# Kernel optimization log

Measured on AMD Instinct MI355X. Metric: run time of the kernel, lower is better.

Reference implementation:

```python
import jax, jax.numpy as jnp
import numpy as np

BOS = 1
MAX_LEN = 20


def _lstm_cell(x, h, c, Wih, Whh, bih, bhh):
    # torch.nn.LSTMCell gate order: i, f, g, o
    g = x @ Wih.T + h @ Whh.T + bih + bhh
    i, f, gg, o = jnp.split(g, 4, axis=-1)
    c = jax.nn.sigmoid(f) * c + jax.nn.sigmoid(i) * jnp.tanh(gg)
    h = jax.nn.sigmoid(o) * jnp.tanh(c)
    return h, c


def setup_inputs() -> dict:
    key = jax.random.key(0)
    ks = jax.random.split(key, 12)
    B, K, D = 512, 36, 2048
    A, H, Em, V = 512, 512, 300, 10000
    s = 0.02
    rn = lambda k, shape, sc=s: sc * jax.random.normal(k, shape, dtype=jnp.float32)
    return {
        'feats': jax.random.normal(ks[0], (B, K, D), dtype=jnp.float32),
        'Wp': rn(ks[1], (A, D)), 'bp': jnp.zeros((A,), jnp.float32),
        'E': rn(ks[2], (V, Em), 0.1).at[0].set(0.0),  # padding_idx = 0
        'Wih1': rn(ks[3], (4 * H, Em + A)), 'Whh1': rn(ks[4], (4 * H, H)),
        'bih1': jnp.zeros((4 * H,), jnp.float32), 'bhh1': jnp.zeros((4 * H,), jnp.float32),
        'Wih2': rn(ks[5], (4 * H, H + A)), 'Whh2': rn(ks[6], (4 * H, H)),
        'bih2': jnp.zeros((4 * H,), jnp.float32), 'bhh2': jnp.zeros((4 * H,), jnp.float32),
        'Wa1': rn(ks[7], (A, H + A)), 'ba1': jnp.zeros((A,), jnp.float32),
        'wa2': rn(ks[8], (1, A)), 'ba2': jnp.zeros((1,), jnp.float32),
        'Wo': rn(ks[9], (V, H)), 'bo': jnp.zeros((V,), jnp.float32),
    }


def reference(feats, Wp, bp, E, Wih1, Whh1, bih1, bhh1, Wih2, Whh2, bih2, bhh2,
              Wa1, ba1, wa2, ba2, Wo, bo):
    B, K, D = feats.shape
    H = Whh1.shape[1]
    f_att = feats @ Wp.T + bp                      # [B, K, A]
    f_mean = f_att.mean(axis=1)                    # [B, A]
    # attn Linear over concat([h1, f_att]): split columns, precompute f_att term
    Wa1_h, Wa1_f = Wa1[:, :H], Wa1[:, H:]
    att_f = f_att @ Wa1_f.T + ba1                  # [B, K, A]
    x0 = jnp.broadcast_to(E[BOS], (B, E.shape[1]))
    z = jnp.zeros((B, H), jnp.float32)
    carry0 = (x0, z, z, z, z)

    def step(carry, _):
        x, h1, c1, h2, c2 = carry
        h1, c1 = _lstm_cell(jnp.concatenate([x, f_mean], axis=-1), h1, c1,
                            Wih1, Whh1, bih1, bhh1)
        pre = jnp.tanh(att_f + (h1 @ Wa1_h.T)[:, None, :])   # [B, K, A]
        e = pre @ wa2[0] + ba2[0]                            # [B, K]
        alpha = jax.nn.softmax(e, axis=-1)
        ctx = jnp.einsum('bk,bka->ba', alpha, f_att)         # [B, A]
        h2, c2 = _lstm_cell(jnp.concatenate([h1, ctx], axis=-1), h2, c2,
                            Wih2, Whh2, bih2, bhh2)
        logit = h2 @ Wo.T + bo                               # [B, V]  (dropout is identity in eval)
        nxt = jnp.argmax(logit, axis=-1)
        return (E[nxt], h1, c1, h2, c2), nxt

    _, ids = jax.lax.scan(step, carry0, None, length=MAX_LEN - 1)
    return ids.T  # [B, MAX_LEN-1], matches torch.stack(out_ids, 1)
```

## Files before the change

### kernel.cpp

```cpp
#include <hip/hip_runtime.h>
#include <math.h>
#include <stdint.h>

constexpr int Bsz = 512, Kf = 36, Dd = 2048, Aa = 512, Hh = 512, Em = 300;
constexpr int Vv = 10000, TSTEPS = 19, BOS = 1;
constexpr int K1 = 832;
constexpr int K2 = 1536;
constexpr int VvP = 10112;
constexpr float SPLIT_S  = 2048.0f;
constexpr float SPLIT_IS = 1.0f / 2048.0f;

#define CDIV(a,b) (((a)+(b)-1)/(b))

typedef _Float16 f16x8 __attribute__((ext_vector_type(8)));
typedef float    f32x4 __attribute__((ext_vector_type(4)));

typedef const unsigned int GU __attribute__((address_space(1)));
typedef unsigned int       LU __attribute__((address_space(3)));

__device__ __forceinline__ void gload16(const void* g, void* l) {
    __builtin_amdgcn_global_load_lds((GU*)g, (LU*)l, 16, 0, 0);
}

template<int N> __device__ __forceinline__ void wait_vm() {
    if constexpr (N == 0)       asm volatile("s_waitcnt vmcnt(0)" ::: "memory");
    else if constexpr (N == 4)  asm volatile("s_waitcnt vmcnt(4)" ::: "memory");
    else if constexpr (N == 6)  asm volatile("s_waitcnt vmcnt(6)" ::: "memory");
    else if constexpr (N == 8)  asm volatile("s_waitcnt vmcnt(8)" ::: "memory");
    else if constexpr (N == 12) asm volatile("s_waitcnt vmcnt(12)" ::: "memory");
    else if constexpr (N == 16) asm volatile("s_waitcnt vmcnt(16)" ::: "memory");
    else static_assert(N == 0, "unsupported vmcnt literal");
}
#define WAIT_LGKM asm volatile("s_waitcnt lgkmcnt(0)" ::: "memory")
#define SB0 __builtin_amdgcn_sched_barrier(0)
#define BAR __builtin_amdgcn_s_barrier()

__device__ __forceinline__ float sigm(float v) { return 1.0f / (1.0f + expf(-v)); }

__device__ __forceinline__ void wsplit(_Float16* __restrict__ hi, _Float16* __restrict__ lo,
                                       size_t idx, float v) {
    _Float16 h = (_Float16)v;
    hi[idx] = h;
    lo[idx] = (_Float16)((v - (float)h) * SPLIT_S);
}

template<int BM, int BN, int BK, bool AF32>
__global__ __launch_bounds__(256)
void gemm_sp(const float* __restrict__ Af,
             const _Float16* __restrict__ Ahi, const _Float16* __restrict__ Alo, int lda,
             const _Float16* __restrict__ Bhi, const _Float16* __restrict__ Blo, int ldb,
             float* __restrict__ C, int ldc, int N, int K,
             const float* __restrict__ bias1, const float* __restrict__ bias2,
             const float* __restrict__ addC)
{
    constexpr int WM = BM / 2, WN = BN / 2;
    constexpr int MF = WM / 16, NF = WN / 16;
    constexpr int PA  = BK / 8;
    constexpr int PSA = BM * 8 + 8;
    constexpr int PSB = BN * 8 + 8;
    constexpr int SZA = PA * PSA, SZB = PA * PSB;
    constexpr int OAH = 0, OAL = SZA, OBH = 2 * SZA, OBL = 2 * SZA + SZB;
    constexpr int BUF = 2 * SZA + 2 * SZB;
    constexpr int NCHA = BM * BK / 2048;
    constexpr int NCHB = BN * BK / 2048;
    constexpr int LW = 2 * NCHA + 2 * NCHB;
    __shared__ _Float16 sm[2 * BUF];

    const int t    = threadIdx.x;
    const int lane = t & 63;
    const int w    = t >> 6;
    const int wr   = w >> 1, wc = w & 1;
    const int m0   = blockIdx.y * BM, n0 = blockIdx.x * BN;
    const int l15  = lane & 15, l4 = lane >> 4;

    f32x4 acch[MF][NF];
    f32x4 accm[MF][NF];
    #pragma unroll
    for (int m = 0; m < MF; ++m)
        #pragma unroll
        for (int n = 0; n < NF; ++n) {
            acch[m][n] = (f32x4){0.f, 0.f, 0.f, 0.f};
            accm[m][n] = (f32x4){0.f, 0.f, 0.f, 0.f};
        }

    const int nkt = K / BK;

    auto stageB = [&](int bufo, int kt) {
        #pragma unroll
        for (int i = 0; i < NCHB; ++i) {
            const int q  = i * 256 + t;
            const int p  = q / BN, r = q % BN;
            const int qw = i * 256 + (t & ~63);
            const int pu = qw / BN, ru = qw % BN;
            const size_t goff = (size_t)(n0 + r) * ldb + kt * BK + p * 8;
            gload16(Bhi + goff, &sm[bufo + OBH + pu * PSB + ru * 8]);
            gload16(Blo + goff, &sm[bufo + OBL + pu * PSB + ru * 8]);
        }
    };
    auto stageA16 = [&](int bufo, int kt) {
        #pragma unroll
        for (int i = 0; i < NCHA; ++i) {
            const int q  = i * 256 + t;
            const int p  = q / BM, r = q % BM;
            const int qw = i * 256 + (t & ~63);
            const int pu = qw / BM, ru = qw % BM;
            const size_t goff = (size_t)(m0 + r) * lda + kt * BK + p * 8;
            gload16(Ahi + goff, &sm[bufo + OAH + pu * PSA + ru * 8]);
            gload16(Alo + goff, &sm[bufo + OAL + pu * PSA + ru * 8]);
        }
    };
    auto issueA = [&](float4 (&rd)[NCHA][2], int kt) {
        #pragma unroll
        for (int i = 0; i < NCHA; ++i) {
            const int q = i * 256 + t;
            const int p = q / BM, r = q % BM;
            const float* src = Af + (size_t)(m0 + r) * lda + kt * BK + p * 8;
            rd[i][0] = *(const float4*)src;
            rd[i][1] = *(const float4*)(src + 4);
        }
    };
    auto writeA = [&](int bufo, float4 (&rd)[NCHA][2]) {
        #pragma unroll
        for (int i = 0; i < NCHA; ++i) {
            const int q = i * 256 + t;
            const int p = q / BM, r = q % BM;
            const float f[8] = {rd[i][0].x, rd[i][0].y, rd[i][0].z, rd[i][0].w,
                                rd[i][1].x, rd[i][1].y, rd[i][1].z, rd[i][1].w};
            f16x8 hi, lo;
            #pragma unroll
            for (int j = 0; j < 8; ++j) {
                _Float16 h = (_Float16)f[j];
                hi[j] = h;
                lo[j] = (_Float16)((f[j] - (float)h) * SPLIT_S);
            }
            *(f16x8*)&sm[bufo + OAH + p * PSA + r * 8] = hi;
            *(f16x8*)&sm[bufo + OAL + p * PSA + r * 8] = lo;
        }
    };
    auto compute = [&](int bufo) {
        #pragma unroll
        for (int s = 0; s < BK / 32; ++s) {
            f16x8 ah[MF], al[MF], bh[NF], bl[NF];
            const int pl = s * 4 + l4;
            #pragma unroll
            for (int m = 0; m < MF; ++m) {
                const int row = wr * WM + m * 16 + l15;
                ah[m] = *(const f16x8*)&sm[bufo + OAH + pl * PSA + row * 8];
                al[m] = *(const f16x8*)&sm[bufo + OAL + pl * PSA + row * 8];
            }
            #pragma unroll
            for (int n = 0; n < NF; ++n) {
                const int row = wc * WN + n * 16 + l15;
                bh[n] = *(const f16x8*)&sm[bufo + OBH + pl * PSB + row * 8];
                bl[n] = *(const f16x8*)&sm[bufo + OBL + pl * PSB + row * 8];
            }
            #pragma unroll
            for (int m = 0; m < MF; ++m)
                #pragma unroll
                for (int n = 0; n < NF; ++n) {
                    acch[m][n] = __builtin_amdgcn_mfma_f32_16x16x32_f16(ah[m], bh[n], acch[m][n], 0, 0, 0);
                    accm[m][n] = __builtin_amdgcn_mfma_f32_16x16x32_f16(ah[m], bl[n], accm[m][n], 0, 0, 0);
                    accm[m][n] = __builtin_amdgcn_mfma_f32_16x16x32_f16(al[m], bh[n], accm[m][n], 0, 0, 0);
                }
        }
    };

    if constexpr (AF32) {
        float4 rA[NCHA][2], rB[NCHA][2];
        issueA(rA, 0); stageB(0, 0);
        for (int kt = 0; kt < nkt; kt += 2) {
            issueA(rB, kt + 1); stageB(BUF, kt + 1);
            wait_vm<LW>(); SB0;
            writeA(0, rA);
            WAIT_LGKM; SB0;
            BAR; SB0;
            compute(0);
            SB0; WAIT_LGKM; BAR; SB0;
            if (kt + 2 < nkt) { issueA(rA, kt + 2); stageB(0, kt + 2); wait_vm<LW>(); }
            else              { wait_vm<0>(); }
            SB0;
            writeA(BUF, rB);
            WAIT_LGKM; SB0;
            BAR; SB0;
            compute(BUF);
            SB0; WAIT_LGKM; BAR; SB0;
        }
    } else {
        stageA16(0, 0); stageB(0, 0);
        for (int kt = 0; kt < nkt; ++kt) {
            const int bufc = (kt & 1) ? BUF : 0;
            const int bufn = BUF - bufc;
            if (kt + 1 < nkt) { stageA16(bufn, kt + 1); stageB(bufn, kt + 1); wait_vm<LW>(); }
            else              { wait_vm<0>(); }
            SB0;
            BAR; SB0;
            compute(bufc);
            SB0; WAIT_LGKM; BAR; SB0;
        }
    }

    #pragma unroll
    for (int m = 0; m < MF; ++m) {
        const int rowb = m0 + wr * WM + m * 16 + l4 * 4;
        #pragma unroll
        for (int n = 0; n < NF; ++n) {
            const int col = n0 + wc * WN + n * 16 + l15;
            if (col < N) {
                float bb = 0.f;
                if (bias1) bb += bias1[col];
                if (bias2) bb += bias2[col];
                #pragma unroll
                for (int r = 0; r < 4; ++r) {
                    const size_t idx = (size_t)(rowb + r) * ldc + col;
                    float v = acch[m][n][r] + accm[m][n][r] * SPLIT_IS + bb;
                    if (addC) v += addC[idx];
                    C[idx] = v;
                }
            }
        }
    }
}

__global__ __launch_bounds__(256)
void split_convert(const float* __restrict__ src, int srcld, int validR,
                   _Float16* __restrict__ dhi, _Float16* __restrict__ dlo,
                   int dstld, int coloff, int R, int C)
{
    const int total = R * C;
    for (int i = blockIdx.x * 256 + threadIdx.x; i < total; i += gridDim.x * 256) {
        const int r = i / C, c = i % C;
        const float v = (r < validR) ? src[(size_t)r * srcld + c] : 0.f;
        wsplit(dhi, dlo, (size_t)r * dstld + coloff + c, v);
    }
}

__global__ __launch_bounds__(256)
void init_kernel(_Float16* __restrict__ a1h, _Float16* __restrict__ a1l,
                 _Float16* __restrict__ a2h, _Float16* __restrict__ a2l,
                 float* __restrict__ c1, float* __restrict__ c2,
                 const float* __restrict__ E)
{
    const int idx = blockIdx.x * 256 + threadIdx.x;
    if (idx < Bsz * K1) {
        const int col = idx % K1;
        const float v = (col < Em) ? E[(size_t)BOS * Em + col] : 0.f;
        wsplit(a1h, a1l, idx, v);
    }
    if (idx < Bsz * K2) wsplit(a2h, a2l, idx, 0.f);
    if (idx < Bsz * Hh) { c1[idx] = 0.f; c2[idx] = 0.f; }
}

__global__ __launch_bounds__(256)
void fmean_kernel(const float* __restrict__ f_att, float* __restrict__ f_mean,
                  _Float16* __restrict__ fmh, _Float16* __restrict__ fml)
{
    const int b = blockIdx.x;
    for (int a = threadIdx.x; a < Aa; a += 256) {
        float s = 0.f;
        for (int k = 0; k < Kf; ++k) s += f_att[((size_t)b * Kf + k) * Aa + a];
        const float v = s * (1.0f / 36.0f);
        f_mean[(size_t)b * Aa + a] = v;
        wsplit(fmh, fml, (size_t)b * Aa + a, v);
    }
}

__global__ __launch_bounds__(256)
void lstm_cell_kernel(const float* __restrict__ g, float* __restrict__ c,
                      _Float16* __restrict__ hhi, _Float16* __restrict__ hlo,
                      int hld, int hoff,
                      _Float16* __restrict__ h2hi, _Float16* __restrict__ h2lo,
                      int h2ld, int h2off)
{
    const int idx = blockIdx.x * 256 + threadIdx.x;
    const int b = idx >> 9, h = idx & 511;
    const float* gb = g + (size_t)b * 2048;
    const float gi = gb[h], gf = gb[512 + h], gc = gb[1024 + h], go = gb[1536 + h];
    const float cv = sigm(gf) * c[idx] + sigm(gi) * tanhf(gc);
    c[idx] = cv;
    const float hv = sigm(go) * tanhf(cv);
    wsplit(hhi, hlo, (size_t)b * hld + hoff + h, hv);
    if (h2hi) wsplit(h2hi, h2lo, (size_t)b * h2ld + h2off + h, hv);
}

__global__ __launch_bounds__(256)
void attn_fused(const float* __restrict__ att_f, const float* __restrict__ q,
                const float* __restrict__ wa2, const float* __restrict__ ba2,
                const float* __restrict__ f_att,
                _Float16* __restrict__ a2h, _Float16* __restrict__ a2l)
{
    const int b = blockIdx.x, tid = threadIdx.x;
    const int w = tid >> 6, lane = tid & 63;
    __shared__ float se[Kf];
    __shared__ float wk[Kf];
    const float* pq = q + (size_t)b * Aa;
    for (int k = w; k < Kf; k += 4) {
        const float* pf = att_f + ((size_t)b * Kf + k) * Aa;
        float s = 0.f;
        #pragma unroll
        for (int j = 0; j < Aa; j += 64) {
            const int a = j + lane;
            s += tanhf(pf[a] + pq[a]) * wa2[a];
        }
        #pragma unroll
        for (int off = 32; off; off >>= 1) s += __shfl_down(s, off);
        if (lane == 0) se[k] = s + ba2[0];
    }
    __syncthreads();
    if (tid < Kf) {
        float mx = -INFINITY;
        for (int k = 0; k < Kf; ++k) mx = fmaxf(mx, se[k]);
        float ssum = 0.f;
        for (int k = 0; k < Kf; ++k) ssum += expf(se[k] - mx);
        wk[tid] = expf(se[tid] - mx) / ssum;
    }
    __syncthreads();
    for (int a = tid; a < Aa; a += 256) {
        float acc = 0.f;
        for (int k = 0; k < Kf; ++k)
            acc = fmaf(wk[k], f_att[((size_t)b * Kf + k) * Aa + a], acc);
        wsplit(a2h, a2l, (size_t)b * K2 + Hh + a, acc);
    }
}

__global__ __launch_bounds__(256)
void argmax_embed_kernel(const float* __restrict__ logits, const float* __restrict__ E,
                         _Float16* __restrict__ a1h, _Float16* __restrict__ a1l,
                         int* __restrict__ out, int t)
{
    const int b = blockIdx.x;
    const int tid = threadIdx.x;
    float best = -INFINITY;
    int bi = Vv;
    for (int j = tid; j < Vv; j += 256) {
        const float v = logits[(size_t)b * Vv + j];
        if (v > best) { best = v; bi = j; }
    }
    __shared__ float sv[256];
    __shared__ int   si[256];
    sv[tid] = best; si[tid] = bi;
    __syncthreads();
    for (int s = 128; s > 0; s >>= 1) {
        if (tid < s) {
            const float v2 = sv[tid + s];
            const int   i2 = si[tid + s];
            if (v2 > sv[tid] || (v2 == sv[tid] && i2 < si[tid])) { sv[tid] = v2; si[tid] = i2; }
        }
        __syncthreads();
    }
    const int idx = si[0];
    if (tid == 0) out[(size_t)b * TSTEPS + t] = idx;
    for (int d = tid; d < Em; d += 256)
        wsplit(a1h, a1l, (size_t)b * K1 + d, E[(size_t)idx * Em + d]);
}

static inline void conv(hipStream_t s, const float* src, int srcld, int validR,
                        _Float16* dhi, _Float16* dlo, int dstld, int coloff, int R, int C)
{
    int blocks = CDIV(R * C, 256); if (blocks > 2048) blocks = 2048;
    split_convert<<<dim3(blocks), dim3(256), 0, s>>>(src, srcld, validR, dhi, dlo, dstld, coloff, R, C);
}

extern "C" void kernel_launch(void* const* d_in, const int* in_sizes, int n_in,
                              void* d_out, int out_size, void* d_ws, size_t ws_size,
                              hipStream_t stream)
{
    const float* feats = (const float*)d_in[0];
    const float* Wp    = (const float*)d_in[1];
    const float* bp    = (const float*)d_in[2];
    const float* E     = (const float*)d_in[3];
    const float* Wih1  = (const float*)d_in[4];
    const float* Whh1  = (const float*)d_in[5];
    const float* bih1  = (const float*)d_in[6];
    const float* bhh1  = (const float*)d_in[7];
    const float* Wih2  = (const float*)d_in[8];
    const float* Whh2  = (const float*)d_in[9];
    const float* bih2  = (const float*)d_in[10];
    const float* bhh2  = (const float*)d_in[11];
    const float* Wa1   = (const float*)d_in[12];
    const float* ba1   = (const float*)d_in[13];
    const float* wa2   = (const float*)d_in[14];
    const float* ba2   = (const float*)d_in[15];
    const float* Wo    = (const float*)d_in[16];
    const float* bo    = (const float*)d_in[17];
    int* out = (int*)d_out;
    (void)in_sizes; (void)n_in; (void)out_size; (void)ws_size;

    uint8_t* w = (uint8_t*)d_ws;
    size_t off = 0;
    auto alloc = [&](size_t bytes) { void* p = w + off; off = (off + bytes + 255) & ~(size_t)255; return p; };

    float*     f_att  = (float*)alloc(18432ull * 512 * 4);
    float*     att_f  = (float*)alloc(18432ull * 512 * 4);
    float*     f_mean = (float*)alloc(512ull * 512 * 4);
    _Float16*  fmh    = (_Float16*)alloc(512ull * 512 * 2);
    _Float16*  fml    = (_Float16*)alloc(512ull * 512 * 2);
    _Float16*  wph    = (_Float16*)alloc(512ull * 2048 * 2);
    _Float16*  wpl    = (_Float16*)alloc(512ull * 2048 * 2);
    _Float16*  w1ph   = (_Float16*)alloc(2048ull * K1 * 2);
    _Float16*  w1pl   = (_Float16*)alloc(2048ull * K1 * 2);
    _Float16*  w1ch   = (_Float16*)alloc(2048ull * 512 * 2);
    _Float16*  w1cl   = (_Float16*)alloc(2048ull * 512 * 2);
    _Float16*  w2ph   = (_Float16*)alloc(2048ull * K2 * 2);
    _Float16*  w2pl   = (_Float16*)alloc(2048ull * K2 * 2);
    _Float16*  wahh   = (_Float16*)alloc(512ull * 512 * 2);
    _Float16*  wahl   = (_Float16*)alloc(512ull * 512 * 2);
    _Float16*  wafh   = (_Float16*)alloc(512ull * 512 * 2);
    _Float16*  wafl   = (_Float16*)alloc(512ull * 512 * 2);
    _Float16*  woh    = (_Float16*)alloc((size_t)VvP * 512 * 2);
    _Float16*  wol    = (_Float16*)alloc((size_t)VvP * 512 * 2);
    float*     g1c    = (float*)alloc(512ull * 2048 * 4);
    _Float16*  a1h    = (_Float16*)alloc(512ull * K1 * 2);
    _Float16*  a1l    = (_Float16*)alloc(512ull * K1 * 2);
    _Float16*  a2h    = (_Float16*)alloc(512ull * K2 * 2);
    _Float16*  a2l    = (_Float16*)alloc(512ull * K2 * 2);
    float*     c1     = (float*)alloc(512ull * 512 * 4);
    float*     c2     = (float*)alloc(512ull * 512 * 4);
    float*     gbuf   = (float*)alloc(512ull * 2048 * 4);
    float*     qbuf   = (float*)alloc(512ull * 512 * 4);
    float*     logits = (float*)alloc(512ull * Vv * 4);

    conv(stream, Wp,          Dd,      512,   wph,  wpl,  2048, 0,    512,  2048);
    conv(stream, Wih1,        Em + Aa, 2048,  w1ph, w1pl, K1,   0,    2048, Em);
    conv(stream, Whh1,        Hh,      2048,  w1ph, w1pl, K1,   Em,   2048, 512);
    conv(stream, Wih1,        Em + Aa, 0,     w1ph, w1pl, K1,   812,  2048, 20);
    conv(stream, Wih1 + Em,   Em + Aa, 2048,  w1ch, w1cl, 512,  0,    2048, 512);
    conv(stream, Wih2,        Hh + Aa, 2048,  w2ph, w2pl, K2,   0,    2048, 1024);
    conv(stream, Whh2,        Hh,      2048,  w2ph, w2pl, K2,   1024, 2048, 512);
    conv(stream, Wa1,         Hh + Aa, 512,   wahh, wahl, 512,  0,    512,  512);
    conv(stream, Wa1 + Hh,    Hh + Aa, 512,   wafh, wafl, 512,  0,    512,  512);
    conv(stream, Wo,          Hh,      Vv,    woh,  wol,  512,  0,    VvP,  512);

    init_kernel<<<dim3(CDIV(Bsz * K2, 256)), dim3(256), 0, stream>>>(a1h, a1l, a2h, a2l, c1, c2, E);

    gemm_sp<128, 128, 32, true><<<dim3(4, 144), 256, 0, stream>>>(
        feats, nullptr, nullptr, Dd, wph, wpl, 2048, f_att, 512, 512, 2048, bp, nullptr, nullptr);
    fmean_kernel<<<dim3(Bsz), dim3(256), 0, stream>>>(f_att, f_mean, fmh, fml);
    gemm_sp<64, 64, 64, false><<<dim3(32, 8), 256, 0, stream>>>(
        nullptr, fmh, fml, 512, w1ch, w1cl, 512, g1c, 2048, 2048, 512, bih1, bhh1, nullptr);
    gemm_sp<128, 128, 32, true><<<dim3(4, 144), 256, 0, stream>>>(
        f_att, nullptr, nullptr, 512, wafh, wafl, 512, att_f, 512, 512, 512, ba1, nullptr, nullptr);

    for (int t = 0; t < TSTEPS; ++t) {
        gemm_sp<64, 64, 64, false><<<dim3(32, 8), 256, 0, stream>>>(
            nullptr, a1h, a1l, K1, w1ph, w1pl, K1, gbuf, 2048, 2048, K1, nullptr, nullptr, g1c);
        lstm_cell_kernel<<<dim3(Bsz * Hh / 256), dim3(256), 0, stream>>>(
            gbuf, c1, a2h, a2l, K2, 0, a1h, a1l, K1, Em);
        gemm_sp<64, 64, 64, false><<<dim3(8, 8), 256, 0, stream>>>(
            nullptr, a2h, a2l, K2, wahh, wahl, 512, qbuf, 512, 512, 512, nullptr, nullptr, nullptr);
        attn_fused<<<dim3(Bsz), dim3(256), 0, stream>>>(att_f, qbuf, wa2, ba2, f_att, a2h, a2l);
        gemm_sp<64, 64, 64, false><<<dim3(32, 8), 256, 0, stream>>>(
            nullptr, a2h, a2l, K2, w2ph, w2pl, K2, gbuf, 2048, 2048, K2, bih2, bhh2, nullptr);
        lstm_cell_kernel<<<dim3(Bsz * Hh / 256), dim3(256), 0, stream>>>(
            gbuf, c2, a2h, a2l, K2, 1024, nullptr, nullptr, 0, 0);
        gemm_sp<64, 64, 64, false><<<dim3(158, 8), 256, 0, stream>>>(
            nullptr, a2h + 1024, a2l + 1024, K2, woh, wol, 512, logits, Vv, Vv, 512, bo, nullptr, nullptr);
        argmax_embed_kernel<<<dim3(Bsz), dim3(256), 0, stream>>>(logits, E, a1h, a1l, out, t);
    }
}
```

Measured before the change: 3.604 ms.

## Fuse vocab argmax into logits GEMM epilogue and retile feature GEMMs with XCD swizzle

The output-projection GEMM no longer writes the full 512x10000 logits matrix. Its epilogue reduces each 64-column tile to a per-row (max, index) candidate using shuffles and shared memory, and the argmax kernel then reduces only 158 candidates per row. This removes the logits store and reload at every decode step. Separately, the two large precompute GEMMs move to 128x64 tiles launched as a 1D swizzled grid with an occupancy hint of 2, which is meant to improve L2 locality across the chiplets. The shared-memory scratch reuse in the epilogue and the tie-breaking toward the lowest index must stay correct.

```diff
diff --git a/kernel.cpp b/kernel.cpp
--- a/kernel.cpp
+++ b/kernel.cpp
@@ -7,6 +7,7 @@
 constexpr int K1 = 832;
 constexpr int K2 = 1536;
 constexpr int VvP = 10112;
+constexpr int NTL = VvP / 64;
 constexpr float SPLIT_S  = 2048.0f;
 constexpr float SPLIT_IS = 1.0f / 2048.0f;
 
@@ -27,8 +28,6 @@
     else if constexpr (N == 4)  asm volatile("s_waitcnt vmcnt(4)" ::: "memory");
     else if constexpr (N == 6)  asm volatile("s_waitcnt vmcnt(6)" ::: "memory");
     else if constexpr (N == 8)  asm volatile("s_waitcnt vmcnt(8)" ::: "memory");
-    else if constexpr (N == 12) asm volatile("s_waitcnt vmcnt(12)" ::: "memory");
-    else if constexpr (N == 16) asm volatile("s_waitcnt vmcnt(16)" ::: "memory");
     else static_assert(N == 0, "unsupported vmcnt literal");
 }
 #define WAIT_LGKM asm volatile("s_waitcnt lgkmcnt(0)" ::: "memory")
@@ -44,14 +43,15 @@
     lo[idx] = (_Float16)((v - (float)h) * SPLIT_S);
 }
 
-template<int BM, int BN, int BK, bool AF32>
-__global__ __launch_bounds__(256)
+template<int BM, int BN, int BK, bool AF32, bool SWZ, int OCC, int EPI>
+__global__ __launch_bounds__(256, OCC)
 void gemm_sp(const float* __restrict__ Af,
              const _Float16* __restrict__ Ahi, const _Float16* __restrict__ Alo, int lda,
              const _Float16* __restrict__ Bhi, const _Float16* __restrict__ Blo, int ldb,
              float* __restrict__ C, int ldc, int N, int K,
              const float* __restrict__ bias1, const float* __restrict__ bias2,
-             const float* __restrict__ addC)
+             const float* __restrict__ addC, int gxn,
+             float* __restrict__ candV, int* __restrict__ candI, int ntl)
 {
     constexpr int WM = BM / 2, WN = BN / 2;
     constexpr int MF = WM / 16, NF = WN / 16;
@@ -66,11 +66,22 @@
     constexpr int LW = 2 * NCHA + 2 * NCHB;
     __shared__ _Float16 sm[2 * BUF];
 
+    int mt, nt;
+    if constexpr (SWZ) {
+        const int nwg = gridDim.x;
+        const int cpx = nwg >> 3;
+        const int orig = blockIdx.x;
+        const int lid = (orig & 7) * cpx + (orig >> 3);
+        nt = lid % gxn; mt = lid / gxn;
+    } else {
+        nt = blockIdx.x; mt = blockIdx.y;
+    }
+    const int m0 = mt * BM, n0 = nt * BN;
+
     const int t    = threadIdx.x;
     const int lane = t & 63;
     const int w    = t >> 6;
     const int wr   = w >> 1, wc = w & 1;
-    const int m0   = blockIdx.y * BM, n0 = blockIdx.x * BN;
     const int l15  = lane & 15, l4 = lane >> 4;
 
     f32x4 acch[MF][NF];
@@ -199,24 +210,78 @@
         }
     }
 
-    #pragma unroll
-    for (int m = 0; m < MF; ++m) {
-        const int rowb = m0 + wr * WM + m * 16 + l4 * 4;
-        #pragma unroll
-        for (int n = 0; n < NF; ++n) {
-            const int col = n0 + wc * WN + n * 16 + l15;
-            if (col < N) {
-                float bb = 0.f;
-                if (bias1) bb += bias1[col];
-                if (bias2) bb += bias2[col];
+    if constexpr (EPI == 0) {
+        #pragma unroll
+        for (int m = 0; m < MF; ++m) {
+            const int rowb = m0 + wr * WM + m * 16 + l4 * 4;
+            #pragma unroll
+            for (int n = 0; n < NF; ++n) {
+                const int col = n0 + wc * WN + n * 16 + l15;
+                if (col < N) {
+                    float bb = 0.f;
+                    if (bias1) bb += bias1[col];
+                    if (bias2) bb += bias2[col];
+                    #pragma unroll
+                    for (int r = 0; r < 4; ++r) {
+                        const size_t idx = (size_t)(rowb + r) * ldc + col;
+                        float v = acch[m][n][r] + accm[m][n][r] * SPLIT_IS + bb;
+                        if (addC) v += addC[idx];
+                        C[idx] = v;
+                    }
+                }
+            }
+        }
+    } else {
+        float* sEv = reinterpret_cast<float*>(&sm[0]);
+        int*   sEi = reinterpret_cast<int*>(&sm[0]) + 2 * BM;
+        float bv[MF][4];
+        int   bix[MF][4];
+        #pragma unroll
+        for (int m = 0; m < MF; ++m)
+            #pragma unroll
+            for (int r = 0; r < 4; ++r) { bv[m][r] = -INFINITY; bix[m][r] = 0x7fffffff; }
+        #pragma unroll
+        for (int m = 0; m < MF; ++m)
+            #pragma unroll
+            for (int r = 0; r < 4; ++r)
+                #pragma unroll
+                for (int n = 0; n < NF; ++n) {
+                    const int col = n0 + wc * WN + n * 16 + l15;
+                    if (col < N) {
+                        const float x = acch[m][n][r] + accm[m][n][r] * SPLIT_IS + bias1[col];
+                        if (x > bv[m][r]) { bv[m][r] = x; bix[m][r] = col; }
+                    }
+                }
+        #pragma unroll
+        for (int mask = 1; mask < 16; mask <<= 1) {
+            #pragma unroll
+            for (int m = 0; m < MF; ++m)
                 #pragma unroll
                 for (int r = 0; r < 4; ++r) {
-                    const size_t idx = (size_t)(rowb + r) * ldc + col;
-                    float v = acch[m][n][r] + accm[m][n][r] * SPLIT_IS + bb;
-                    if (addC) v += addC[idx];
-                    C[idx] = v;
+                    const float ov = __shfl_xor(bv[m][r], mask);
+                    const int   oi = __shfl_xor(bix[m][r], mask);
+                    if (ov > bv[m][r] || (ov == bv[m][r] && oi < bix[m][r])) {
+                        bv[m][r] = ov; bix[m][r] = oi;
+                    }
                 }
-            }
+        }
+        if (l15 == 0) {
+            #pragma unroll
+            for (int m = 0; m < MF; ++m)
+                #pragma unroll
+                for (int r = 0; r < 4; ++r) {
+                    const int rl = wr * WM + m * 16 + l4 * 4 + r;
+                    sEv[wc * BM + rl] = bv[m][r];
+                    sEi[wc * BM + rl] = bix[m][r];
+                }
+        }
+        __syncthreads();
+        if (t < BM) {
+            float v0 = sEv[t]; int i0 = sEi[t];
+            const float v1 = sEv[BM + t]; const int i1 = sEi[BM + t];
+            if (v1 > v0 || (v1 == v0 && i1 < i0)) { v0 = v1; i0 = i1; }
+            candV[(size_t)(m0 + t) * ntl + nt] = v0;
+            candI[(size_t)(m0 + t) * ntl + nt] = i0;
         }
     }
 }
@@ -323,21 +388,18 @@
 }
 
 __global__ __launch_bounds__(256)
-void argmax_embed_kernel(const float* __restrict__ logits, const float* __restrict__ E,
+void argmax_embed_kernel(const float* __restrict__ candV, const int* __restrict__ candI,
+                         const float* __restrict__ E,
                          _Float16* __restrict__ a1h, _Float16* __restrict__ a1l,
-                         int* __restrict__ out, int t)
+                         int* __restrict__ out, int t, int ntl)
 {
     const int b = blockIdx.x;
     const int tid = threadIdx.x;
-    float best = -INFINITY;
-    int bi = Vv;
-    for (int j = tid; j < Vv; j += 256) {
-        const float v = logits[(size_t)b * Vv + j];
-        if (v > best) { best = v; bi = j; }
-    }
     __shared__ float sv[256];
     __shared__ int   si[256];
-    sv[tid] = best; si[tid] = bi;
+    float bvv = -INFINITY; int bii = 0x7fffffff;
+    if (tid < ntl) { bvv = candV[(size_t)b * ntl + tid]; bii = candI[(size_t)b * ntl + tid]; }
+    sv[tid] = bvv; si[tid] = bii;
     __syncthreads();
     for (int s = 128; s > 0; s >>= 1) {
         if (tid < s) {
@@ -417,43 +479,53 @@
     float*     c2     = (float*)alloc(512ull * 512 * 4);
     float*     gbuf   = (float*)alloc(512ull * 2048 * 4);
     float*     qbuf   = (float*)alloc(512ull * 512 * 4);
-    float*     logits = (float*)alloc(512ull * Vv * 4);
-
-    conv(stream, Wp,          Dd,      512,   wph,  wpl,  2048, 0,    512,  2048);
-    conv(stream, Wih1,        Em + Aa, 2048,  w1ph, w1pl, K1,   0,    2048, Em);
-    conv(stream, Whh1,        Hh,      2048,  w1ph, w1pl, K1,   Em,   2048, 512);
-    conv(stream, Wih1,        Em + Aa, 0,     w1ph, w1pl, K1,   812,  2048, 20);
-    conv(stream, Wih1 + Em,   Em + Aa, 2048,  w1ch, w1cl, 512,  0,    2048, 512);
-    conv(stream, Wih2,        Hh + Aa, 2048,  w2ph, w2pl, K2,   0,    2048, 1024);
-    conv(stream, Whh2,        Hh,      2048,  w2ph, w2pl, K2,   1024, 2048, 512);
-    conv(stream, Wa1,         Hh + Aa, 512,   wahh, wahl, 512,  0,    512,  512);
-    conv(stream, Wa1 + Hh,    Hh + Aa, 512,   wafh, wafl, 512,  0,    512,  512);
-    conv(stream, Wo,          Hh,      Vv,    woh,  wol,  512,  0,    VvP,  512);
+    float*     candV  = (float*)alloc(512ull * NTL * 4);
+    int*       candI  = (int*)alloc(512ull * NTL * 4);
+
+    conv(stream, Wp,        Dd,      512,  wph,  wpl,  2048, 0,    512,  2048);
+    conv(stream, Wih1,      Em + Aa, 2048, w1ph, w1pl, K1,   0,    2048, Em);
+    conv(stream, Whh1,      Hh,      2048, w1ph, w1pl, K1,   Em,   2048, 512);
+    conv(stream, Wih1,      Em + Aa, 0,    w1ph, w1pl, K1,   812,  2048, 20);
+    conv(stream, Wih1 + Em, Em + Aa, 2048, w1ch, w1cl, 512,  0,    2048, 512);
+    conv(stream, Wih2,      Hh + Aa, 2048, w2ph, w2pl, K2,   0,    2048, 1024);
+    conv(stream, Whh2,      Hh,      2048, w2ph, w2pl, K2,   1024, 2048, 512);
+    conv(stream, Wa1,       Hh + Aa, 512,  wahh, wahl, 512,  0,    512,  512);
+    conv(stream, Wa1 + Hh,  Hh + Aa, 512,  wafh, wafl, 512,  0,    512,  512);
+    conv(stream, Wo,        Hh,      Vv,   woh,  wol,  512,  0,    VvP,  512);
 
     init_kernel<<<dim3(CDIV(Bsz * K2, 256)), dim3(256), 0, stream>>>(a1h, a1l, a2h, a2l, c1, c2, E);
 
-    gemm_sp<128, 128, 32, true><<<dim3(4, 144), 256, 0, stream>>>(
-        feats, nullptr, nullptr, Dd, wph, wpl, 2048, f_att, 512, 512, 2048, bp, nullptr, nullptr);
+    gemm_sp<128, 64, 32, true, true, 2, 0><<<dim3(1152), 256, 0, stream>>>(
+        feats, nullptr, nullptr, Dd, wph, wpl, 2048, f_att, 512, 512, 2048,
+        bp, nullptr, nullptr, 8, nullptr, nullptr, 0);
     fmean_kernel<<<dim3(Bsz), dim3(256), 0, stream>>>(f_att, f_mean, fmh, fml);
-    gemm_sp<64, 64, 64, false><<<dim3(32, 8), 256, 0, stream>>>(
-        nullptr, fmh, fml, 512, w1ch, w1cl, 512, g1c, 2048, 2048, 512, bih1, bhh1, nullptr);
-    gemm_sp<128, 128, 32, true><<<dim3(4, 144), 256, 0, stream>>>(
-        f_att, nullptr, nullptr, 512, wafh, wafl, 512, att_f, 512, 512, 512, ba1, nullptr, nullptr);
+    gemm_sp<64, 64, 64, false, false, 1, 0><<<dim3(32, 8), 256, 0, stream>>>(
+        nullptr, fmh, fml, 512, w1ch, w1cl, 512, g1c, 2048, 2048, 512,
+        bih1, bhh1, nullptr, 0, nullptr, nullptr, 0);
+    gemm_sp<128, 64, 32, true, true, 2, 0><<<dim3(1152), 256, 0, stream>>>(
+        f_att, nullptr, nullptr, 512, wafh, wafl, 512, att_f, 512, 512, 512,
+        ba1, nullptr, nullptr, 8, nullptr, nullptr, 0);
 
     for (int t = 0; t < TSTEPS; ++t) {
-        gemm_sp<64, 64, 64, false><<<dim3(32, 8), 256, 0, stream>>>(
-            nullptr, a1h, a1l, K1, w1ph, w1pl, K1, gbuf, 2048, 2048, K1, nullptr, nullptr, g1c);
+        gemm_sp<64, 64, 64, false, false, 1, 0><<<dim3(32, 8), 256, 0, stream>>>(
+            nullptr, a1h, a1l, K1, w1ph, w1pl, K1, gbuf, 2048, 2048, K1,
+            nullptr, nullptr, g1c, 0, nullptr, nullptr, 0);
         lstm_cell_kernel<<<dim3(Bsz * Hh / 256), dim3(256), 0, stream>>>(
             gbuf, c1, a2h, a2l, K2, 0, a1h, a1l, K1, Em);
-        gemm_sp<64, 64, 64, false><<<dim3(8, 8), 256, 0, stream>>>(
-            nullptr, a2h, a2l, K2, wahh, wahl, 512, qbuf, 512, 512, 512, nullptr, nullptr, nullptr);
-        attn_fused<<<dim3(Bsz), dim3(256), 0, stream>>>(att_f, qbuf, wa2, ba2, f_att, a2h, a2l);
-        gemm_sp<64, 64, 64, false><<<dim3(32, 8), 256, 0, stream>>>(
-            nullptr, a2h, a2l, K2, w2ph, w2pl, K2, gbuf, 2048, 2048, K2, bih2, bhh2, nullptr);
+        gemm_sp<64, 64, 64, false, false, 1, 0><<<dim3(8, 8), 256, 0, stream>>>(
+            nullptr, a2h, a2l, K2, wahh, wahl, 512, qbuf, 512, 512, 512,
+            nullptr, nullptr, nullptr, 0, nullptr, nullptr, 0);
+        attn_fused<<<dim3(Bsz), dim3(256), 0, stream>>>(
+            att_f, qbuf, wa2, ba2, f_att, a2h, a2l);
+        gemm_sp<64, 64, 64, false, false, 1, 0><<<dim3(32, 8), 256, 0, stream>>>(
+            nullptr, a2h, a2l, K2, w2ph, w2pl, K2, gbuf, 2048, 2048, K2,
+            bih2, bhh2, nullptr, 0, nullptr, nullptr, 0);
         lstm_cell_kernel<<<dim3(Bsz * Hh / 256), dim3(256), 0, stream>>>(
             gbuf, c2, a2h, a2l, K2, 1024, nullptr, nullptr, 0, 0);
-        gemm_sp<64, 64, 64, false><<<dim3(158, 8), 256, 0, stream>>>(
-            nullptr, a2h + 1024, a2l + 1024, K2, woh, wol, 512, logits, Vv, Vv, 512, bo, nullptr, nullptr);
-        argmax_embed_kernel<<<dim3(Bsz), dim3(256), 0, stream>>>(logits, E, a1h, a1l, out, t);
-    }
-}
+        gemm_sp<64, 64, 64, false, false, 1, 3><<<dim3(NTL, 8), 256, 0, stream>>>(
+            nullptr, a2h + 1024, a2l + 1024, K2, woh, wol, 512, nullptr, 0, Vv, 512,
+            bo, nullptr, nullptr, 0, candV, candI, NTL);
+        argmax_embed_kernel<<<dim3(Bsz), dim3(256), 0, stream>>>(
+            candV, candI, E, a1h, a1l, out, t, NTL);
+    }
+}
```

Measured after the change: 3.485 ms. 3.3% less time.
